# Performance work log

Measured on AMD Instinct MI355X. Metric: run time of the kernel, lower is better.

The kernel has to match this reference:

```python
import jax, jax.numpy as jnp
import numpy as np

NL = 8      # num layers (['self','cross']*4)
H = 8       # heads
EPS = 1e-5  # torch LayerNorm default


def _layernorm(x, g, b):
    mu = jnp.mean(x, axis=-1, keepdims=True)
    var = jnp.mean((x - mu) ** 2, axis=-1, keepdims=True)
    return (x - mu) * jax.lax.rsqrt(var + EPS) * g + b


def _encoder_layer(x, source, Wq, Wk, Wv, Wm, W1, W2, g1, b1, g2, b2):
    # x: [N, L, C], source: [N, S, C]
    N, L, C = x.shape
    D = C // H
    q = (x @ Wq).reshape(N, L, H, D)
    k = (source @ Wk).reshape(N, -1, H, D)
    v = (source @ Wv).reshape(N, -1, H, D)
    # naive full attention: explicit [N, L, S, H] scores (as in FullAttention)
    qk = jnp.einsum('nlhd,nshd->nlsh', q, k)
    A = jax.nn.softmax(qk * (1.0 / np.sqrt(D)), axis=2)
    msg = jnp.einsum('nlsh,nshd->nlhd', A, v).reshape(N, L, C)
    msg = _layernorm(msg @ Wm, g1, b1)
    m = jnp.concatenate([x, msg], axis=-1)          # [N, L, 2C]
    m = jax.nn.relu(m @ W1) @ W2                    # [N, L, C]
    m = _layernorm(m, g2, b2)
    return x + m


def _loftr(feat0, feat1, Wq, Wk, Wv, Wm, W1, W2, g1, b1, g2, b2):
    names = ['self', 'cross'] * 4
    for i, name in enumerate(names):
        p = (Wq[i], Wk[i], Wv[i], Wm[i], W1[i], W2[i], g1[i], b1[i], g2[i], b2[i])
        if name == 'self':
            feat0 = _encoder_layer(feat0, feat0, *p)
            feat1 = _encoder_layer(feat1, feat1, *p)
        else:  # cross; note feat0 is updated before being fed to feat1's layer
            feat0 = _encoder_layer(feat0, feat1, *p)
            feat1 = _encoder_layer(feat1, feat0, *p)
    return jnp.stack([feat0, feat1], axis=0)  # [2, N, L, C]


def setup_inputs() -> dict:
    key = jax.random.key(0)
    ks = jax.random.split(key, 10)
    N, L, C = 8, 1024, 768
    s = 1.0 / np.sqrt(C)       # xavier-ish scale for [C, C]
    s2 = 1.0 / np.sqrt(2 * C)  # for MLP fan-in 2C
    return {
        'feat0': jax.random.normal(ks[0], (N, L, C), jnp.float32),
        'feat1': jax.random.normal(ks[1], (N, L, C), jnp.float32),
        'Wq': jax.random.normal(ks[2], (NL, C, C), jnp.float32) * s,
        'Wk': jax.random.normal(ks[3], (NL, C, C), jnp.float32) * s,
        'Wv': jax.random.normal(ks[4], (NL, C, C), jnp.float32) * s,
        'Wm': jax.random.normal(ks[5], (NL, C, C), jnp.float32) * s,
        'W1': jax.random.normal(ks[6], (NL, 2 * C, 2 * C), jnp.float32) * s2,
        'W2': jax.random.normal(ks[7], (NL, 2 * C, C), jnp.float32) * s2,
        'g1': jnp.ones((NL, C), jnp.float32),
        'b1': jnp.zeros((NL, C), jnp.float32),
        'g2': jnp.ones((NL, C), jnp.float32),
        'b2': jnp.zeros((NL, C), jnp.float32),
    }


def reference(feat0, feat1, Wq, Wk, Wv, Wm, W1, W2, g1, b1, g2, b2):
    return _loftr(feat0, feat1, Wq, Wk, Wv, Wm, W1, W2, g1, b1, g2, b2)
```

## Files before the change

kernel.cpp:

```cpp
#include <hip/hip_runtime.h>
#include <hip/hip_bf16.h>

typedef __hip_bfloat16 bf16;
typedef __bf16 bf16x8 __attribute__((ext_vector_type(8)));
typedef float f32x4 __attribute__((ext_vector_type(4)));

#define AS1 __attribute__((address_space(1)))
#define AS3 __attribute__((address_space(3)))
__device__ __forceinline__ void gl_lds16(const void* g, void* l) {
    __builtin_amdgcn_global_load_lds((const AS1 void*)g, (AS3 void*)l, 16, 0, 0);
}

__device__ __forceinline__ float fexp2(float x) {
#if __has_builtin(__builtin_amdgcn_exp2f)
    return __builtin_amdgcn_exp2f(x);
#else
    return exp2f(x);
#endif
}

__device__ __forceinline__ int xcd_swz(int did, int nwg) {
    return (did & 7) * (nwg >> 3) + (did >> 3);
}


__global__ __launch_bounds__(256) void cvt_f32_bf16_k(const float* __restrict__ in, bf16* __restrict__ out,
                                                      int ostride, int total)
{
    int i = blockIdx.x * 256 + threadIdx.x;
    int e = i * 4;
    if (e >= total) return;
    int row = e / 768;
    int col = e - row * 768;
    const float4 f = *(const float4*)(in + e);
    bf16 o4[4];
    o4[0] = __float2bfloat16(f.x); o4[1] = __float2bfloat16(f.y);
    o4[2] = __float2bfloat16(f.z); o4[3] = __float2bfloat16(f.w);
    *(uint2*)(out + (size_t)row * ostride + col) = *(uint2*)o4;
}

__global__ void transpose_cvt_k(const float* __restrict__ in, bf16* __restrict__ out, int R, int C,
                                float scale, size_t lstride)
{
    __shared__ float t[32][33];
    const int tx = threadIdx.x, ty = threadIdx.y;
    in  += (size_t)blockIdx.z * R * C;
    out += (size_t)blockIdx.z * lstride;
    const int c0 = blockIdx.x * 32, r0 = blockIdx.y * 32;
    #pragma unroll
    for (int i = 0; i < 4; ++i)
        t[ty + i*8][tx] = in[(size_t)(r0 + ty + i*8) * C + c0 + tx];
    __syncthreads();
    #pragma unroll
    for (int i = 0; i < 4; ++i)
        out[(size_t)(c0 + ty + i*8) * R + r0 + tx] = __float2bfloat16(t[tx][ty + i*8] * scale);
}

template<int EPI>
__global__ __launch_bounds__(256) void gemm_bt_k(const bf16* __restrict__ A, int lda,
                                                 const bf16* __restrict__ BT, int K,
                                                 void* __restrict__ Cp, int ldc, int colshift,
                                                 bf16* __restrict__ Ck, bf16* __restrict__ Cv)
{
    __shared__ bf16 a_sm[2][4096];
    __shared__ bf16 b_sm[2][4096];
    const int tid = threadIdx.x;
    const int lane = tid & 63;
    const int wid = tid >> 6;
    const int wr = wid >> 1, wc = wid & 1;

    const int nwg = gridDim.x * gridDim.y;
    const int did = blockIdx.x + gridDim.x * blockIdx.y;
    const int wgid = xcd_swz(did, nwg);
    const int row0 = (wgid % gridDim.x) * 128;
    const int col0 = (wgid / gridDim.x) * 128;
    const int g = lane >> 4, r16 = lane & 15;

    const int r4 = lane >> 2;
    const int sc = (lane & 3) ^ ((lane >> 3) & 3);
    const bf16* gA[2]; const bf16* gB[2]; int loff[2];
    #pragma unroll
    for (int i = 0; i < 2; ++i) {
        const int blk = wid*2 + i;
        gA[i] = A  + (size_t)(row0 + blk*16 + r4) * lda + sc*8;
        gB[i] = BT + (size_t)(col0 + blk*16 + r4) * K   + sc*8;
        loff[i] = blk * 512;
    }
    const int foff = r16*32 + ((g ^ ((r16 >> 1) & 3)) * 8);

    f32x4 acc[4][4];
    #pragma unroll
    for (int m = 0; m < 4; ++m)
        #pragma unroll
        for (int n = 0; n < 4; ++n)
            #pragma unroll
            for (int r = 0; r < 4; ++r) acc[m][n][r] = 0.f;

    #pragma unroll
    for (int i = 0; i < 2; ++i) {
        gl_lds16(gA[i], &a_sm[0][loff[i]]);
        gl_lds16(gB[i], &b_sm[0][loff[i]]);
    }
    __syncthreads();

    int cur = 0;
    for (int k0 = 0; k0 < K; k0 += 32) {
        if (k0 + 32 < K) {
            #pragma unroll
            for (int i = 0; i < 2; ++i) {
                gl_lds16(gA[i] + k0 + 32, &a_sm[cur ^ 1][loff[i]]);
                gl_lds16(gB[i] + k0 + 32, &b_sm[cur ^ 1][loff[i]]);
            }
        }
        bf16x8 af[4], bfr[4];
        #pragma unroll
        for (int m = 0; m < 4; ++m) af[m]  = *(const bf16x8*)&a_sm[cur][(wr*4 + m)*512 + foff];
        #pragma unroll
        for (int n = 0; n < 4; ++n) bfr[n] = *(const bf16x8*)&b_sm[cur][(wc*4 + n)*512 + foff];
        __builtin_amdgcn_s_setprio(1);
        #pragma unroll
        for (int m = 0; m < 4; ++m)
            #pragma unroll
            for (int n = 0; n < 4; ++n)
                acc[m][n] = __builtin_amdgcn_mfma_f32_16x16x32_bf16(af[m], bfr[n], acc[m][n], 0, 0, 0);
        __builtin_amdgcn_s_setprio(0);
        __syncthreads();
        cur ^= 1;
    }

    #pragma unroll
    for (int m = 0; m < 4; ++m) {
        const int orow = row0 + wr*64 + m*16 + g*4;
        #pragma unroll
        for (int n = 0; n < 4; ++n) {
            const int ocol = col0 + wc*64 + n*16 + r16;
            if (EPI == 4 || EPI == 5) {
                const int ce = ocol + colshift;
                const int seg = ce / 768;
                const int ci = ce - seg*768;
                if (seg <= 1) {
                    bf16* dst = (seg == 0) ? (bf16*)Cp : Ck;
                    #pragma unroll
                    for (int r = 0; r < 4; ++r)
                        dst[(size_t)(orow + r)*768 + ci] = __float2bfloat16(acc[m][n][r]);
                } else {
                    const int nn = orow >> 10, ss = orow & 1023;
                    const int hh = ci / 96, dd = ci - hh * 96;
                    bf16 pk[4];
                    #pragma unroll
                    for (int r = 0; r < 4; ++r) pk[r] = __float2bfloat16(acc[m][n][r]);
                    *(uint2*)&Cv[(((size_t)nn*8 + hh)*96 + dd)*1024 + ss] = *(uint2*)pk;
                }
            } else {
                #pragma unroll
                for (int r = 0; r < 4; ++r) {
                    float v = acc[m][n][r];
                    if (EPI == 1) v = fmaxf(v, 0.f);
                    if (EPI == 2) ((float*)Cp)[(size_t)(orow + r)*ldc + ocol] = v;
                    else          ((bf16*)Cp) [(size_t)(orow + r)*ldc + ocol] = __float2bfloat16(v);
                }
            }
        }
    }
}

__global__ __launch_bounds__(512) void attn_k(const bf16* __restrict__ qb, const bf16* __restrict__ kb,
                                              const bf16* __restrict__ vtb, bf16* __restrict__ msgb)
{
    __shared__ bf16 kv_sm[2][12*512];
    __shared__ bf16 p_sm_all[8][32][40];
    const int tid = threadIdx.x;
    const int lane = tid & 63;
    const int w = tid >> 6;
    const int g = lane >> 4, r16 = lane & 15;

    const int nwg = gridDim.x * gridDim.y;
    const int did = blockIdx.x + gridDim.x * blockIdx.y;
    const int wgid = xcd_swz(did, nwg);
    const int qx = wgid % gridDim.x;
    const int nh = wgid / gridDim.x;
    const int n = nh >> 3, h = nh & 7;
    const int q0 = qx * 256 + w * 32;

    bf16 (*p_sm)[40] = p_sm_all[w];

    const bf16* kbase = kb  + ((size_t)n*1024)*768 + (size_t)h*96;
    const bf16* vbase = vtb + ((size_t)(n*8 + h))*96*1024;

    bf16x8 aq[2][3];
    #pragma unroll
    for (int qh = 0; qh < 2; ++qh) {
        const size_t qoff = ((size_t)n*1024 + q0 + qh*16 + r16) * 768 + (size_t)h*96;
        #pragma unroll
        for (int c = 0; c < 3; ++c) aq[qh][c] = *(const bf16x8*)&qb[qoff + c*32 + g*8];
    }

    const int r4 = lane >> 2;
    const int sc = (lane & 3) ^ ((lane >> 3) & 3);
    const bf16* gsrc[2]; size_t gstep[2]; int dstoff[2];
    const int nissue = (w < 4) ? 2 : 1;
    #pragma unroll
    for (int jj = 0; jj < 2; ++jj) {
        const int issue = w + jj*8;
        if (issue < 6) {
            const int c = issue >> 1, kh = issue & 1;
            gsrc[jj]  = kbase + (size_t)(kh*16 + r4)*768 + c*32 + sc*8;
            gstep[jj] = 768;
        } else {
            gsrc[jj]  = vbase + (size_t)((issue-6)*16 + r4)*1024 + sc*8;
            gstep[jj] = 1;
        }
        dstoff[jj] = (issue < 12) ? issue * 512 : 0;
    }
    const int foff = r16*32 + ((g ^ ((r16 >> 1) & 3)) * 8);

    float m_run[2], l_run[2];
    #pragma unroll
    for (int qh = 0; qh < 2; ++qh) { m_run[qh] = -1e30f; l_run[qh] = 0.f; }
    f32x4 o[2][6];
    #pragma unroll
    for (int qg = 0; qg < 2; ++qg)
        #pragma unroll
        for (int f = 0; f < 6; ++f)
            #pragma unroll
            for (int r = 0; r < 4; ++r) o[qg][f][r] = 0.f;

    int cur = 0;
    gl_lds16(gsrc[0], &kv_sm[0][dstoff[0]]);
    if (nissue == 2) gl_lds16(gsrc[1], &kv_sm[0][dstoff[1]]);
    __syncthreads();

    for (int kt = 0; kt < 1024; kt += 32) {
        if (kt + 32 < 1024) {
            gl_lds16(gsrc[0] + (size_t)(kt + 32) * gstep[0], &kv_sm[cur ^ 1][dstoff[0]]);
            if (nissue == 2) gl_lds16(gsrc[1] + (size_t)(kt + 32) * gstep[1], &kv_sm[cur ^ 1][dstoff[1]]);
        }
        const bf16* rd = kv_sm[cur];

        f32x4 s[2][2];
        #pragma unroll
        for (int kh = 0; kh < 2; ++kh)
            #pragma unroll
            for (int qh = 0; qh < 2; ++qh)
                #pragma unroll
                for (int r = 0; r < 4; ++r) s[kh][qh][r] = 0.f;
        __builtin_amdgcn_s_setprio(1);
        #pragma unroll
        for (int c = 0; c < 3; ++c) {
            bf16x8 ak0 = *(const bf16x8*)&rd[(c*2 + 0)*512 + foff];
            bf16x8 ak1 = *(const bf16x8*)&rd[(c*2 + 1)*512 + foff];
            s[0][0] = __builtin_amdgcn_mfma_f32_16x16x32_bf16(ak0, aq[0][c], s[0][0], 0, 0, 0);
            s[0][1] = __builtin_amdgcn_mfma_f32_16x16x32_bf16(ak0, aq[1][c], s[0][1], 0, 0, 0);
            s[1][0] = __builtin_amdgcn_mfma_f32_16x16x32_bf16(ak1, aq[0][c], s[1][0], 0, 0, 0);
            s[1][1] = __builtin_amdgcn_mfma_f32_16x16x32_bf16(ak1, aq[1][c], s[1][1], 0, 0, 0);
        }
        __builtin_amdgcn_s_setprio(0);

        float pmv[2], gr[2];
        #pragma unroll
        for (int qh = 0; qh < 2; ++qh) {
            float pm = fmaxf(fmaxf(fmaxf(s[0][qh][0], s[0][qh][1]), fmaxf(s[0][qh][2], s[0][qh][3])),
                             fmaxf(fmaxf(s[1][qh][0], s[1][qh][1]), fmaxf(s[1][qh][2], s[1][qh][3])));
            pm = fmaxf(pm, __shfl_xor(pm, 16, 64));
            pm = fmaxf(pm, __shfl_xor(pm, 32, 64));
            pmv[qh] = pm;
            gr[qh] = pm - m_run[qh];
        }
        if (__any(fmaxf(gr[0], gr[1]) > 8.0f)) {
            float alpha_c[2];
            #pragma unroll
            for (int qh = 0; qh < 2; ++qh) {
                float mn = fmaxf(m_run[qh], pmv[qh]);
                alpha_c[qh] = fexp2(m_run[qh] - mn);
                m_run[qh] = mn;
                l_run[qh] *= alpha_c[qh];
            }
            #pragma unroll
            for (int qg = 0; qg < 2; ++qg)
                #pragma unroll
                for (int r = 0; r < 4; ++r) {
                    float ar = __shfl(alpha_c[qg], g*4 + r, 64);
                    #pragma unroll
                    for (int f = 0; f < 6; ++f) o[qg][f][r] *= ar;
                }
        }
        #pragma unroll
        for (int qh = 0; qh < 2; ++qh) {
            bf16 pk0[4], pk1[4];
            float rs = 0.f;
            #pragma unroll
            for (int r = 0; r < 4; ++r) {
                float p0 = fexp2(s[0][qh][r] - m_run[qh]);
                float p1 = fexp2(s[1][qh][r] - m_run[qh]);
                rs += p0 + p1;
                pk0[r] = __float2bfloat16(p0);
                pk1[r] = __float2bfloat16(p1);
            }
            rs += __shfl_xor(rs, 16, 64);
            rs += __shfl_xor(rs, 32, 64);
            l_run[qh] += rs;
            *(uint2*)&p_sm[qh*16 + r16][g*4]      = *(uint2*)pk0;
            *(uint2*)&p_sm[qh*16 + r16][16 + g*4] = *(uint2*)pk1;
        }

        bf16x8 pa0 = *(const bf16x8*)&p_sm[r16][g*8];
        bf16x8 pa1 = *(const bf16x8*)&p_sm[16 + r16][g*8];
        __builtin_amdgcn_s_setprio(1);
        #pragma unroll
        for (int f = 0; f < 6; ++f) {
            bf16x8 bv = *(const bf16x8*)&rd[(6 + f)*512 + foff];
            o[0][f] = __builtin_amdgcn_mfma_f32_16x16x32_bf16(pa0, bv, o[0][f], 0, 0, 0);
            o[1][f] = __builtin_amdgcn_mfma_f32_16x16x32_bf16(pa1, bv, o[1][f], 0, 0, 0);
        }
        __builtin_amdgcn_s_setprio(0);

        __syncthreads();
        cur ^= 1;
    }

    float linv[2][4];
    #pragma unroll
    for (int qg = 0; qg < 2; ++qg)
        #pragma unroll
        for (int r = 0; r < 4; ++r)
            linv[qg][r] = 1.0f / __shfl(l_run[qg], g*4 + r, 64);

    #pragma unroll
    for (int qg = 0; qg < 2; ++qg) {
        const size_t obase = ((size_t)n*1024 + q0 + qg*16 + g*4) * 768 + (size_t)h*96;
        #pragma unroll
        for (int f = 0; f < 6; ++f)
            #pragma unroll
            for (int r = 0; r < 4; ++r)
                msgb[obase + (size_t)r*768 + f*16 + r16] = __float2bfloat16(o[qg][f][r] * linv[qg][r]);
    }
}

template<int MODE>
__global__ __launch_bounds__(256) void ln_k(const float* __restrict__ in, const float* __restrict__ g,
                                            const float* __restrict__ b, bf16* __restrict__ outc,
                                            float* __restrict__ x)
{
    const int row = blockIdx.x;
    const int tid = threadIdx.x;
    const float* rp = in + (size_t)row * 768;
    float v[3];
    #pragma unroll
    for (int j = 0; j < 3; ++j) v[j] = rp[tid + j*256];
    float s  = v[0] + v[1] + v[2];
    float sq = v[0]*v[0] + v[1]*v[1] + v[2]*v[2];
    #pragma unroll
    for (int off = 32; off >= 1; off >>= 1) {
        s  += __shfl_xor(s,  off, 64);
        sq += __shfl_xor(sq, off, 64);
    }
    __shared__ float red[2][4];
    const int wid = tid >> 6;
    if ((tid & 63) == 0) { red[0][wid] = s; red[1][wid] = sq; }
    __syncthreads();
    const float S  = red[0][0] + red[0][1] + red[0][2] + red[0][3];
    const float SQ = red[1][0] + red[1][1] + red[1][2] + red[1][3];
    const float mu = S * (1.f/768.f);
    float var = SQ * (1.f/768.f) - mu*mu;
    var = fmaxf(var, 0.f);
    const float rs = rsqrtf(var + 1e-5f);
    #pragma unroll
    for (int j = 0; j < 3; ++j) {
        const int c = tid + j*256;
        const float y = (v[j] - mu) * rs * g[c] + b[c];
        if (MODE == 1) {
            outc[(size_t)row*1536 + 768 + c] = __float2bfloat16(y);
        } else {
            const float nx = x[(size_t)row*768 + c] + y;
            x[(size_t)row*768 + c] = nx;
            outc[(size_t)row*1536 + c] = __float2bfloat16(nx);
        }
    }
}

extern "C" void kernel_launch(void* const* d_in, const int* in_sizes, int n_in,
                              void* d_out, int out_size, void* d_ws, size_t ws_size,
                              hipStream_t stream)
{
    const float* feat0 = (const float*)d_in[0];
    const float* feat1 = (const float*)d_in[1];
    const float* Wq = (const float*)d_in[2];
    const float* Wk = (const float*)d_in[3];
    const float* Wv = (const float*)d_in[4];
    const float* Wm = (const float*)d_in[5];
    const float* W1 = (const float*)d_in[6];
    const float* W2 = (const float*)d_in[7];
    const float* g1 = (const float*)d_in[8];
    const float* b1 = (const float*)d_in[9];
    const float* g2 = (const float*)d_in[10];
    const float* b2 = (const float*)d_in[11];

    char* p = (char*)d_ws;
    auto take = [&](size_t bytes) { char* q = p; p += (bytes + 255) & ~(size_t)255; return q; };
    bf16* wqkvT = (bf16*)take((size_t)8*2304*768*2);
    bf16* wmT = (bf16*)take((size_t)8*768*768*2);
    bf16* w1T = (bf16*)take((size_t)8*1536*1536*2);
    bf16* w2T = (bf16*)take((size_t)8*768*1536*2);
    bf16* concat0 = (bf16*)take((size_t)8192*1536*2);
    bf16* concat1 = (bf16*)take((size_t)8192*1536*2);
    bf16* qb   = (bf16*)take((size_t)8192*768*2);
    bf16* kb   = (bf16*)take((size_t)8192*768*2);
    bf16* vtb  = (bf16*)take((size_t)8192*768*2);
    bf16* m1b  = (bf16*)take((size_t)8192*1536*2);
    float* t0  = (float*)take((size_t)8192*768*4);
    bf16* msgb = qb;

    float* x0 = (float*)d_out;
    float* x1 = x0 + (size_t)8192*768;

    hipMemcpyAsync(x0, feat0, (size_t)8192*768*4, hipMemcpyDeviceToDevice, stream);
    hipMemcpyAsync(x1, feat1, (size_t)8192*768*4, hipMemcpyDeviceToDevice, stream);

    const float s_qk = 0.14724444f;
    const dim3 tb(32, 8);
    const size_t QKV = (size_t)2304*768;
    transpose_cvt_k<<<dim3(24,24,8), tb, 0, stream>>>(Wq, wqkvT,            768, 768,  s_qk, QKV);
    transpose_cvt_k<<<dim3(24,24,8), tb, 0, stream>>>(Wk, wqkvT + 768*768,  768, 768,  1.0f, QKV);
    transpose_cvt_k<<<dim3(24,24,8), tb, 0, stream>>>(Wv, wqkvT + 1536*768, 768, 768,  1.0f, QKV);
    transpose_cvt_k<<<dim3(24,24,8), tb, 0, stream>>>(Wm, wmT, 768, 768,  1.0f, (size_t)768*768);
    transpose_cvt_k<<<dim3(48,48,8), tb, 0, stream>>>(W1, w1T, 1536, 1536, 1.0f, (size_t)1536*1536);
    transpose_cvt_k<<<dim3(24,48,8), tb, 0, stream>>>(W2, w2T, 1536, 768,  1.0f, (size_t)1536*768);

    const int total = 8192*768;
    cvt_f32_bf16_k<<<6144, 256, 0, stream>>>(feat0, concat0, 1536, total);
    cvt_f32_bf16_k<<<6144, 256, 0, stream>>>(feat1, concat1, 1536, total);

    auto encode = [&](float* x, bf16* cS, const bf16* cR, int i, bool self) {
        const bf16* wl = wqkvT + (size_t)i * QKV;
        if (self) {
            gemm_bt_k<4><<<dim3(64,18), 256, 0, stream>>>(cS, 1536, wl, 768, qb, 768, 0, kb, vtb);
        } else {
            gemm_bt_k<0><<<dim3(64,6),  256, 0, stream>>>(cS, 1536, wl, 768, qb, 768, 0, nullptr, nullptr);
            gemm_bt_k<5><<<dim3(64,12), 256, 0, stream>>>(cR, 1536, wl + (size_t)768*768, 768,
                                                          nullptr, 0, 768, kb, vtb);
        }
        attn_k<<<dim3(4,64), 512, 0, stream>>>(qb, kb, vtb, msgb);
        gemm_bt_k<2><<<dim3(64,6),  256, 0, stream>>>(msgb, 768, wmT + (size_t)i*768*768, 768,
                                                      t0, 768, 0, nullptr, nullptr);
        ln_k<1><<<8192, 256, 0, stream>>>(t0, g1 + i*768, b1 + i*768, cS, nullptr);
        gemm_bt_k<1><<<dim3(64,12), 256, 0, stream>>>(cS, 1536, w1T + (size_t)i*1536*1536, 1536,
                                                      m1b, 1536, 0, nullptr, nullptr);
        gemm_bt_k<2><<<dim3(64,6),  256, 0, stream>>>(m1b, 1536, w2T + (size_t)i*768*1536, 1536,
                                                      t0, 768, 0, nullptr, nullptr);
        ln_k<2><<<8192, 256, 0, stream>>>(t0, g2 + i*768, b2 + i*768, cS, x);
    };

    for (int i = 0; i < 8; ++i) {
        if ((i & 1) == 0) { encode(x0, concat0, concat0, i, true);  encode(x1, concat1, concat1, i, true); }
        else              { encode(x0, concat0, concat1, i, false); encode(x1, concat1, concat0, i, false); }
    }
}
```

Baseline: 4.044 ms.

## Triple-buffer LDS loads with one barrier per k-step in GEMM and attention

Moves the GEMM and attention K/V global-to-LDS loads from double to triple buffering. Each iteration now waits with explicit vmcnt counts and a single s_barrier, then prefetches two tiles ahead. This keeps more memory traffic in flight and removes the trailing __syncthreads per step. The GEMM tile index mapping is also swapped to walk columns fastest for better cache locality. The cost is 50% more LDS per block, which may lower occupancy, and correctness now depends on the hand-written waitcnt values.

```diff
diff --git a/kernel.cpp b/kernel.cpp
--- a/kernel.cpp
+++ b/kernel.cpp
@@ -62,8 +62,8 @@
                                                  void* __restrict__ Cp, int ldc, int colshift,
                                                  bf16* __restrict__ Ck, bf16* __restrict__ Cv)
 {
-    __shared__ bf16 a_sm[2][4096];
-    __shared__ bf16 b_sm[2][4096];
+    __shared__ bf16 a_sm[3][4096];
+    __shared__ bf16 b_sm[3][4096];
     const int tid = threadIdx.x;
     const int lane = tid & 63;
     const int wid = tid >> 6;
@@ -72,8 +72,8 @@
     const int nwg = gridDim.x * gridDim.y;
     const int did = blockIdx.x + gridDim.x * blockIdx.y;
     const int wgid = xcd_swz(did, nwg);
-    const int row0 = (wgid % gridDim.x) * 128;
-    const int col0 = (wgid / gridDim.x) * 128;
+    const int col0 = (wgid % gridDim.y) * 128;
+    const int row0 = (wgid / gridDim.y) * 128;
     const int g = lane >> 4, r16 = lane & 15;
 
     const int r4 = lane >> 2;
@@ -98,18 +98,25 @@
 
     #pragma unroll
     for (int i = 0; i < 2; ++i) {
-        gl_lds16(gA[i], &a_sm[0][loff[i]]);
-        gl_lds16(gB[i], &b_sm[0][loff[i]]);
-    }
-    __syncthreads();
-
-    int cur = 0;
+        gl_lds16(gA[i],      &a_sm[0][loff[i]]);
+        gl_lds16(gB[i],      &b_sm[0][loff[i]]);
+    }
+    #pragma unroll
+    for (int i = 0; i < 2; ++i) {
+        gl_lds16(gA[i] + 32, &a_sm[1][loff[i]]);
+        gl_lds16(gB[i] + 32, &b_sm[1][loff[i]]);
+    }
+
+    int cur = 0, pre = 2;
     for (int k0 = 0; k0 < K; k0 += 32) {
-        if (k0 + 32 < K) {
+        if (k0 + 32 < K) asm volatile("s_waitcnt vmcnt(4)" ::: "memory");
+        else             asm volatile("s_waitcnt vmcnt(0)" ::: "memory");
+        __builtin_amdgcn_s_barrier();
+        if (k0 + 64 < K) {
             #pragma unroll
             for (int i = 0; i < 2; ++i) {
-                gl_lds16(gA[i] + k0 + 32, &a_sm[cur ^ 1][loff[i]]);
-                gl_lds16(gB[i] + k0 + 32, &b_sm[cur ^ 1][loff[i]]);
+                gl_lds16(gA[i] + k0 + 64, &a_sm[pre][loff[i]]);
+                gl_lds16(gB[i] + k0 + 64, &b_sm[pre][loff[i]]);
             }
         }
         bf16x8 af[4], bfr[4];
@@ -117,6 +124,7 @@
         for (int m = 0; m < 4; ++m) af[m]  = *(const bf16x8*)&a_sm[cur][(wr*4 + m)*512 + foff];
         #pragma unroll
         for (int n = 0; n < 4; ++n) bfr[n] = *(const bf16x8*)&b_sm[cur][(wc*4 + n)*512 + foff];
+        asm volatile("s_waitcnt lgkmcnt(0)" ::: "memory");
         __builtin_amdgcn_s_setprio(1);
         #pragma unroll
         for (int m = 0; m < 4; ++m)
@@ -124,8 +132,8 @@
             for (int n = 0; n < 4; ++n)
                 acc[m][n] = __builtin_amdgcn_mfma_f32_16x16x32_bf16(af[m], bfr[n], acc[m][n], 0, 0, 0);
         __builtin_amdgcn_s_setprio(0);
-        __syncthreads();
-        cur ^= 1;
+        cur = (cur == 2) ? 0 : cur + 1;
+        pre = (pre == 2) ? 0 : pre + 1;
     }
 
     #pragma unroll
@@ -167,7 +175,7 @@
 __global__ __launch_bounds__(512) void attn_k(const bf16* __restrict__ qb, const bf16* __restrict__ kb,
                                               const bf16* __restrict__ vtb, bf16* __restrict__ msgb)
 {
-    __shared__ bf16 kv_sm[2][12*512];
+    __shared__ bf16 kv_sm[3][12*512];
     __shared__ bf16 p_sm_all[8][32][40];
     const int tid = threadIdx.x;
     const int lane = tid & 63;
@@ -225,15 +233,23 @@
             #pragma unroll
             for (int r = 0; r < 4; ++r) o[qg][f][r] = 0.f;
 
-    int cur = 0;
     gl_lds16(gsrc[0], &kv_sm[0][dstoff[0]]);
     if (nissue == 2) gl_lds16(gsrc[1], &kv_sm[0][dstoff[1]]);
-    __syncthreads();
-
+    gl_lds16(gsrc[0] + 32 * gstep[0], &kv_sm[1][dstoff[0]]);
+    if (nissue == 2) gl_lds16(gsrc[1] + 32 * gstep[1], &kv_sm[1][dstoff[1]]);
+
+    int cur = 0, pre = 2;
     for (int kt = 0; kt < 1024; kt += 32) {
         if (kt + 32 < 1024) {
-            gl_lds16(gsrc[0] + (size_t)(kt + 32) * gstep[0], &kv_sm[cur ^ 1][dstoff[0]]);
-            if (nissue == 2) gl_lds16(gsrc[1] + (size_t)(kt + 32) * gstep[1], &kv_sm[cur ^ 1][dstoff[1]]);
+            if (nissue == 2) asm volatile("s_waitcnt vmcnt(2)" ::: "memory");
+            else             asm volatile("s_waitcnt vmcnt(1)" ::: "memory");
+        } else {
+            asm volatile("s_waitcnt vmcnt(0)" ::: "memory");
+        }
+        __builtin_amdgcn_s_barrier();
+        if (kt + 64 < 1024) {
+            gl_lds16(gsrc[0] + (size_t)(kt + 64) * gstep[0], &kv_sm[pre][dstoff[0]]);
+            if (nissue == 2) gl_lds16(gsrc[1] + (size_t)(kt + 64) * gstep[1], &kv_sm[pre][dstoff[1]]);
         }
         const bf16* rd = kv_sm[cur];
 
@@ -313,9 +329,9 @@
             o[1][f] = __builtin_amdgcn_mfma_f32_16x16x32_bf16(pa1, bv, o[1][f], 0, 0, 0);
         }
         __builtin_amdgcn_s_setprio(0);
-
-        __syncthreads();
-        cur ^= 1;
+        asm volatile("s_waitcnt lgkmcnt(0)" ::: "memory");
+        cur = (cur == 2) ? 0 : cur + 1;
+        pre = (pre == 2) ? 0 : pre + 1;
     }
 
     float linv[2][4];
```

Result: faster. 3.809 ms (-5.8%).
